# Kernel optimization log

Measured on AMD Instinct MI355X. Metric: run time of the kernel, lower is better.

Reference implementation:

```python
import jax, jax.numpy as jnp
import numpy as np
from functools import partial

TAU = 2.0
V_TH = 1.0
ALPHA = 2.0  # spikingjelly surrogate.ATan default alpha
EPS = 1e-5   # nn.LayerNorm default eps

@jax.custom_vjp
def atan_spike(v):
    # Heaviside forward; ATan surrogate gradient in bwd.
    return (v >= 0.0).astype(v.dtype)

def _atan_fwd(v):
    return atan_spike(v), v

def _atan_bwd(v, g):
    sg = (ALPHA / 2.0) / (1.0 + (jnp.pi / 2.0 * ALPHA * v) ** 2)
    return (g * sg,)

atan_spike.defvjp(_atan_fwd, _atan_bwd)

def lif_multi_step(x):
    # x: [B, T, H]; LIF with decay_input=True, v_reset=0 (hard reset), detach_reset=True.
    xt = jnp.swapaxes(x, 0, 1)  # [T, B, H]
    v0 = jnp.zeros(x.shape[:1] + x.shape[2:], dtype=x.dtype)  # reset_net per call
    def step(v, x_t):
        v = v + (x_t - v) / TAU            # charge
        s = atan_spike(v - V_TH)           # fire (surrogate grad)
        v = v * (1.0 - jax.lax.stop_gradient(s))  # hard reset to 0, detached spike
        return v, s
    _, spikes = jax.lax.scan(step, v0, xt)
    return jnp.swapaxes(spikes, 0, 1)  # [B, T, H]

def layer_norm(x, gamma, beta):
    mu = jnp.mean(x, axis=-1, keepdims=True)
    var = jnp.mean((x - mu) ** 2, axis=-1, keepdims=True)
    return (x - mu) * jax.lax.rsqrt(var + EPS) * gamma + beta

def setup_inputs() -> dict:
    key = jax.random.key(0)
    ks = jax.random.split(key, 5)
    B, T, D, H = 64, 1024, 256, 512
    x = jax.random.normal(ks[0], (B, T, D), dtype=jnp.float32)
    sc1 = 1.0 / np.sqrt(D)
    sc2 = 1.0 / np.sqrt(H)
    W1 = jax.random.uniform(ks[1], (H, D), jnp.float32, -sc1, sc1)
    b1 = jax.random.uniform(ks[2], (H,), jnp.float32, -sc1, sc1)
    W2 = jax.random.uniform(ks[3], (D, H), jnp.float32, -sc2, sc2)
    b2 = jax.random.uniform(ks[4], (D,), jnp.float32, -sc2, sc2)
    g1 = jnp.ones((H,), jnp.float32); be1 = jnp.zeros((H,), jnp.float32)
    g2 = jnp.ones((D,), jnp.float32); be2 = jnp.zeros((D,), jnp.float32)
    return {"x": x, "W1": W1, "b1": b1, "g1": g1, "be1": be1,
            "W2": W2, "b2": b2, "g2": g2, "be2": be2}

def reference(x, W1, b1, g1, be1, W2, b2, g2, be2):
    residual = x
    h = jnp.einsum('btd,hd->bth', x, W1) + b1   # fc1
    h = layer_norm(h, g1, be1)                   # norm1
    h = lif_multi_step(h)                        # lif1 (dropout = identity, eval)
    y = jnp.einsum('bth,dh->btd', h, W2) + b2    # fc2
    y = layer_norm(y, g2, be2)                   # norm2
    y = lif_multi_step(y)                        # lif2
    return residual + y
```

## Files before the change

kernel.cpp:

```cpp
#include <hip/hip_runtime.h>

typedef int v4i  __attribute__((ext_vector_type(4)));
typedef int v16i __attribute__((ext_vector_type(16)));

#define TT 1024
#define DD 256
#define HH 512
#define CB 32
#define CM (CB*TT)

__device__ __forceinline__ double shfl_xor_d(double x, int m) {
    union { double d; int u[2]; } a; a.d = x;
    a.u[0] = __shfl_xor(a.u[0], m);
    a.u[1] = __shfl_xor(a.u[1], m);
    return a.d;
}

__global__ __launch_bounds__(256) void prep_w_k(const float* __restrict__ W1,
                                                const float* __restrict__ W2,
                                                signed char* __restrict__ W1p,
                                                signed char* __restrict__ W2p) {
    int i = blockIdx.x * 256 + threadIdx.x;
    {
        double a = (double)W1[i];
        double inv = 1024.0, s = 1.0 / 1024.0;
#pragma unroll
        for (int p = 0; p < 5; ++p) {
            int d = (int)(a * inv);
            a -= d * s;
            W1p[(size_t)p * 131072 + i] = (signed char)d;
            inv *= 128.0; s *= (1.0 / 128.0);
        }
    }
    {
        double a = (double)W2[i];
        double inv = 1024.0, s = 1.0 / 1024.0;
#pragma unroll
        for (int p = 0; p < 5; ++p) {
            int d = (int)(a * inv);
            a -= d * s;
            W2p[(size_t)p * 131072 + i] = (signed char)d;
            inv *= 128.0; s *= (1.0 / 128.0);
        }
    }
}

__global__ __launch_bounds__(256) void split_x_k(const float* __restrict__ xc,
                                                 signed char* __restrict__ Xp) {
    int gid = blockIdx.x * 256 + threadIdx.x;
    int e0 = gid * 4;
    float4 xv = *(const float4*)(xc + e0);
    float fa[4] = {xv.x, xv.y, xv.z, xv.w};
    int dg[4][5];
#pragma unroll
    for (int e = 0; e < 4; ++e) {
        double a = (double)fa[e];
        double inv = 8.0, s = 0.125;
#pragma unroll
        for (int p = 0; p < 5; ++p) {
            int d = (int)(a * inv);
            a -= d * s;
            dg[e][p] = d;
            inv *= 128.0; s *= (1.0 / 128.0);
        }
    }
#pragma unroll
    for (int p = 0; p < 5; ++p) {
        int pk = (dg[0][p] & 255) | ((dg[1][p] & 255) << 8) |
                 ((dg[2][p] & 255) << 16) | ((dg[3][p] & 255) << 24);
        *(int*)(Xp + (size_t)p * ((size_t)CM * 256) + e0) = pk;
    }
}

__global__ __launch_bounds__(512, 2) void gemm1_i8(
    const signed char* __restrict__ Xp, const signed char* __restrict__ W1p,
    const float* __restrict__ b1, const float* __restrict__ g1,
    const float* __restrict__ be1, double* __restrict__ Hn) {
    __shared__ signed char Asm[5 * 32 * 256];
    __shared__ signed char Bsm[2][512 * 80];
    __shared__ double RS[8][32], RQ[8][32];
    __shared__ double MUs[32], IVs[32];

    const int tid = threadIdx.x;
    const int wave = tid >> 6, lane = tid & 63, lrow = lane & 31, lhalf = lane >> 5;
    const int m0 = blockIdx.x * 32;

    v16i acc[5][2];
#pragma unroll
    for (int g = 0; g < 5; ++g)
#pragma unroll
        for (int nt = 0; nt < 2; ++nt)
#pragma unroll
            for (int r = 0; r < 16; ++r) acc[g][nt][r] = 0;

#pragma unroll
    for (int t = 0; t < 5; ++t) {
        int idx = tid + t * 512;
        int p = idx >> 9, r = (idx >> 4) & 31, k16 = (idx & 15) << 4;
        v4i v = *(const v4i*)(Xp + (size_t)p * ((size_t)CM * 256) +
                              (size_t)(m0 + r) * 256 + k16);
        *(v4i*)&Asm[p * 8192 + r * 256 + (k16 ^ ((r & 7) << 4))] = v;
    }

    v4i breg[4];
    {
        const signed char* bp = W1p + (size_t)tid * 256;
#pragma unroll
        for (int q = 0; q < 4; ++q) breg[q] = *(const v4i*)(bp + q * 16);
    }

#pragma unroll
    for (int j = 0; j < 5; ++j) {
#pragma unroll
        for (int kk = 0; kk < 4; ++kk) {
            const int it = j * 4 + kk, bb = it & 1;
            __syncthreads();
#pragma unroll
            for (int q = 0; q < 4; ++q)
                *(v4i*)&Bsm[bb][tid * 80 + ((q * 16) ^ ((tid & 3) << 4))] = breg[q];
            __syncthreads();
            if (it < 19) {
                const int nj = (kk == 3) ? j + 1 : j;
                const int nkk = (kk == 3) ? 0 : kk + 1;
                const signed char* bp = W1p + (size_t)nj * 131072 +
                                        (size_t)tid * 256 + nkk * 64;
#pragma unroll
                for (int q = 0; q < 4; ++q) breg[q] = *(const v4i*)(bp + q * 16);
            }
            v4i bf[2][2];
#pragma unroll
            for (int nt = 0; nt < 2; ++nt)
#pragma unroll
                for (int ks = 0; ks < 2; ++ks) {
                    int hcol = wave * 64 + nt * 32 + lrow;
                    int kl = ks * 32 + lhalf * 16;
                    bf[nt][ks] = *(const v4i*)&Bsm[bb][hcol * 80 + (kl ^ ((hcol & 3) << 4))];
                }
#pragma unroll
            for (int i = 0; i <= 4 - j; ++i) {
                v4i af[2];
#pragma unroll
                for (int ks = 0; ks < 2; ++ks) {
                    int k = kk * 64 + ks * 32 + lhalf * 16;
                    af[ks] = *(const v4i*)&Asm[i * 8192 + lrow * 256 + (k ^ ((lrow & 7) << 4))];
                }
#pragma unroll
                for (int nt = 0; nt < 2; ++nt)
#pragma unroll
                    for (int ks = 0; ks < 2; ++ks)
                        acc[i + j][nt] = __builtin_amdgcn_mfma_i32_32x32x32_i8(
                            af[ks], bf[nt][ks], acc[i + j][nt], 0, 0, 0);
            }
        }
    }

    const double scl[5] = {0x1p-13, 0x1p-20, 0x1p-27, 0x1p-34, 0x1p-41};
    double vv[2][16];
    int colc[2];
#pragma unroll
    for (int nt = 0; nt < 2; ++nt) {
        colc[nt] = wave * 64 + nt * 32 + lrow;
        double bcol = (double)b1[colc[nt]];
#pragma unroll
        for (int r = 0; r < 16; ++r) {
            double t = 0.0;
#pragma unroll
            for (int g = 0; g < 5; ++g) t = fma((double)acc[g][nt][r], scl[g], t);
            vv[nt][r] = t + bcol;
        }
    }
    double ps[16], pq[16];
#pragma unroll
    for (int r = 0; r < 16; ++r) {
        ps[r] = vv[0][r] + vv[1][r];
        pq[r] = vv[0][r] * vv[0][r] + vv[1][r] * vv[1][r];
    }
#pragma unroll
    for (int m = 1; m < 32; m <<= 1)
#pragma unroll
        for (int r = 0; r < 16; ++r) {
            ps[r] += shfl_xor_d(ps[r], m);
            pq[r] += shfl_xor_d(pq[r], m);
        }
    if (lrow == 0) {
#pragma unroll
        for (int r = 0; r < 16; ++r) {
            int rw = (r & 3) + 8 * (r >> 2) + 4 * lhalf;
            RS[wave][rw] = ps[r];
            RQ[wave][rw] = pq[r];
        }
    }
    __syncthreads();
    if (tid < 32) {
        double s = 0.0, q = 0.0;
#pragma unroll
        for (int w = 0; w < 8; ++w) { s += RS[w][tid]; q += RQ[w][tid]; }
        double mu = s * (1.0 / 512.0);
        double var = q * (1.0 / 512.0) - mu * mu;
        MUs[tid] = mu;
        IVs[tid] = 1.0 / sqrt(var + 1e-5);
    }
    __syncthreads();
#pragma unroll
    for (int nt = 0; nt < 2; ++nt) {
        int col = colc[nt];
        double gg = (double)g1[col], bb2 = (double)be1[col];
#pragma unroll
        for (int r = 0; r < 16; ++r) {
            int rw = (r & 3) + 8 * (r >> 2) + 4 * lhalf;
            double o = (vv[nt][r] - MUs[rw]) * IVs[rw] * gg + bb2;
            Hn[(size_t)(m0 + rw) * 512 + col] = o;
        }
    }
}

__global__ __launch_bounds__(512, 2) void gemm2_i8(
    const signed char* __restrict__ S, const signed char* __restrict__ W2p,
    const float* __restrict__ b2, const float* __restrict__ g2,
    const float* __restrict__ be2, double* __restrict__ Yn) {
    __shared__ signed char Asm[64 * 512];
    __shared__ signed char Bsm[2][256 * 144];
    __shared__ double RS[4][64], RQ[4][64];
    __shared__ double MUs[64], IVs[64];

    const int tid = threadIdx.x;
    const int wave = tid >> 6, lane = tid & 63, lrow = lane & 31, lhalf = lane >> 5;
    const int wm = wave >> 2, wn = wave & 3;
    const int m0 = blockIdx.x * 64;

    v16i acc[5][2];
#pragma unroll
    for (int g = 0; g < 5; ++g)
#pragma unroll
        for (int nt = 0; nt < 2; ++nt)
#pragma unroll
            for (int r = 0; r < 16; ++r) acc[g][nt][r] = 0;

    {
        int r = tid >> 3, k0 = (tid & 7) * 64;
#pragma unroll
        for (int q = 0; q < 4; ++q) {
            int k = k0 + q * 16;
            v4i v = *(const v4i*)(S + (size_t)(m0 + r) * 512 + k);
            *(v4i*)&Asm[r * 512 + (k ^ ((r & 7) << 4))] = v;
        }
    }

    v4i breg[4];
    {
        const signed char* bp = W2p + (size_t)(tid >> 1) * 512 + (tid & 1) * 64;
#pragma unroll
        for (int q = 0; q < 4; ++q) breg[q] = *(const v4i*)(bp + q * 16);
    }

#pragma unroll
    for (int j = 0; j < 5; ++j) {
#pragma unroll
        for (int kk = 0; kk < 4; ++kk) {
            const int it = j * 4 + kk, bb = it & 1;
            const int d = tid >> 1, klb = (tid & 1) * 64;
            __syncthreads();
#pragma unroll
            for (int q = 0; q < 4; ++q) {
                int kl = klb + q * 16;
                *(v4i*)&Bsm[bb][d * 144 + (kl ^ ((d & 7) << 4))] = breg[q];
            }
            __syncthreads();
            if (it < 19) {
                const int nj = (kk == 3) ? j + 1 : j;
                const int nkk = (kk == 3) ? 0 : kk + 1;
                const signed char* bp = W2p + (size_t)nj * 131072 +
                                        (size_t)(tid >> 1) * 512 + nkk * 128 + (tid & 1) * 64;
#pragma unroll
                for (int q = 0; q < 4; ++q) breg[q] = *(const v4i*)(bp + q * 16);
            }
            v4i bf[2][4];
#pragma unroll
            for (int nt = 0; nt < 2; ++nt)
#pragma unroll
                for (int ks = 0; ks < 4; ++ks) {
                    int dcol = wn * 64 + nt * 32 + lrow;
                    int kl = ks * 32 + lhalf * 16;
                    bf[nt][ks] = *(const v4i*)&Bsm[bb][dcol * 144 + (kl ^ ((dcol & 7) << 4))];
                }
            v4i af[4];
#pragma unroll
            for (int ks = 0; ks < 4; ++ks) {
                int arow = wm * 32 + lrow;
                int k = kk * 128 + ks * 32 + lhalf * 16;
                af[ks] = *(const v4i*)&Asm[arow * 512 + (k ^ ((arow & 7) << 4))];
            }
#pragma unroll
            for (int nt = 0; nt < 2; ++nt)
#pragma unroll
                for (int ks = 0; ks < 4; ++ks)
                    acc[j][nt] = __builtin_amdgcn_mfma_i32_32x32x32_i8(
                        af[ks], bf[nt][ks], acc[j][nt], 0, 0, 0);
        }
    }

    const double scl[5] = {0x1p-10, 0x1p-17, 0x1p-24, 0x1p-31, 0x1p-38};
    double vv[2][16];
    int colc[2];
#pragma unroll
    for (int nt = 0; nt < 2; ++nt) {
        colc[nt] = wn * 64 + nt * 32 + lrow;
        double bcol = (double)b2[colc[nt]];
#pragma unroll
        for (int r = 0; r < 16; ++r) {
            double t = 0.0;
#pragma unroll
            for (int g = 0; g < 5; ++g) t = fma((double)acc[g][nt][r], scl[g], t);
            vv[nt][r] = t + bcol;
        }
    }
    double ps[16], pq[16];
#pragma unroll
    for (int r = 0; r < 16; ++r) {
        ps[r] = vv[0][r] + vv[1][r];
        pq[r] = vv[0][r] * vv[0][r] + vv[1][r] * vv[1][r];
    }
#pragma unroll
    for (int m = 1; m < 32; m <<= 1)
#pragma unroll
        for (int r = 0; r < 16; ++r) {
            ps[r] += shfl_xor_d(ps[r], m);
            pq[r] += shfl_xor_d(pq[r], m);
        }
    if (lrow == 0) {
#pragma unroll
        for (int r = 0; r < 16; ++r) {
            int rw = wm * 32 + (r & 3) + 8 * (r >> 2) + 4 * lhalf;
            RS[wn][rw] = ps[r];
            RQ[wn][rw] = pq[r];
        }
    }
    __syncthreads();
    if (tid < 64) {
        double s = 0.0, q = 0.0;
#pragma unroll
        for (int w = 0; w < 4; ++w) { s += RS[w][tid]; q += RQ[w][tid]; }
        double mu = s * (1.0 / 256.0);
        double var = q * (1.0 / 256.0) - mu * mu;
        MUs[tid] = mu;
        IVs[tid] = 1.0 / sqrt(var + 1e-5);
    }
    __syncthreads();
#pragma unroll
    for (int nt = 0; nt < 2; ++nt) {
        int col = colc[nt];
        double gg = (double)g2[col], bb2 = (double)be2[col];
#pragma unroll
        for (int r = 0; r < 16; ++r) {
            int rw = wm * 32 + (r & 3) + 8 * (r >> 2) + 4 * lhalf;
            double o = (vv[nt][r] - MUs[rw]) * IVs[rw] * gg + bb2;
            Yn[(size_t)(m0 + rw) * 256 + col] = o;
        }
    }
}

__global__ __launch_bounds__(64) void lif1_k(const double* __restrict__ Hn,
                                             signed char* __restrict__ S) {
    int b = blockIdx.x >> 3;
    int h = (blockIdx.x & 7) * 64 + threadIdx.x;
    const double* src = Hn + (size_t)b * TT * HH + h;
    signed char* dst = S + (size_t)b * TT * HH + h;
    double v = 0.0;
    double buf[4][16];
#pragma unroll
    for (int gg = 0; gg < 3; ++gg)
#pragma unroll
        for (int t = 0; t < 16; ++t) buf[gg][t] = src[(size_t)(gg * 16 + t) * HH];
    for (int g4 = 0; g4 < 64; g4 += 4) {
#pragma unroll
        for (int u = 0; u < 4; ++u) {
            int g = g4 + u;
            if (g + 3 < 64) {
#pragma unroll
                for (int t = 0; t < 16; ++t)
                    buf[(u + 3) & 3][t] = src[(size_t)((g + 3) * 16 + t) * HH];
            }
#pragma unroll
            for (int t = 0; t < 16; ++t) {
                v += (buf[u][t] - v) * 0.5;
                bool sp = (v >= 1.0);
                dst[(size_t)(g * 16 + t) * HH] = sp ? 1 : 0;
                if (sp) v = 0.0;
            }
        }
    }
}

__global__ __launch_bounds__(64) void lif2_k(const double* __restrict__ Yn,
                                             const float* __restrict__ X,
                                             float* __restrict__ out) {
    int b = blockIdx.x >> 2;
    int d = (blockIdx.x & 3) * 64 + threadIdx.x;
    const double* src = Yn + (size_t)b * TT * DD + d;
    const float* xs = X + (size_t)b * TT * DD + d;
    float* dst = out + (size_t)b * TT * DD + d;
    double v = 0.0;
    double bufy[4][16];
    float bufx[4][16];
#pragma unroll
    for (int gg = 0; gg < 3; ++gg)
#pragma unroll
        for (int t = 0; t < 16; ++t) {
            bufy[gg][t] = src[(size_t)(gg * 16 + t) * DD];
            bufx[gg][t] = xs[(size_t)(gg * 16 + t) * DD];
        }
    for (int g4 = 0; g4 < 64; g4 += 4) {
#pragma unroll
        for (int u = 0; u < 4; ++u) {
            int g = g4 + u;
            if (g + 3 < 64) {
#pragma unroll
                for (int t = 0; t < 16; ++t) {
                    bufy[(u + 3) & 3][t] = src[(size_t)((g + 3) * 16 + t) * DD];
                    bufx[(u + 3) & 3][t] = xs[(size_t)((g + 3) * 16 + t) * DD];
                }
            }
#pragma unroll
            for (int t = 0; t < 16; ++t) {
                v += (bufy[u][t] - v) * 0.5;
                bool sp = (v >= 1.0);
                dst[(size_t)(g * 16 + t) * DD] = bufx[u][t] + (sp ? 1.0f : 0.0f);
                if (sp) v = 0.0;
            }
        }
    }
}

extern "C" void kernel_launch(void* const* d_in, const int* in_sizes, int n_in,
                              void* d_out, int out_size, void* d_ws, size_t ws_size,
                              hipStream_t stream) {
    const float* x   = (const float*)d_in[0];
    const float* W1  = (const float*)d_in[1];
    const float* b1  = (const float*)d_in[2];
    const float* g1  = (const float*)d_in[3];
    const float* be1 = (const float*)d_in[4];
    const float* W2  = (const float*)d_in[5];
    const float* b2  = (const float*)d_in[6];
    const float* g2  = (const float*)d_in[7];
    const float* be2 = (const float*)d_in[8];
    float* out = (float*)d_out;

    char* ws = (char*)d_ws;
    signed char* W1p = (signed char*)ws;
    signed char* W2p = (signed char*)(ws + (1ull << 20));
    signed char* Xp  = (signed char*)(ws + (2ull << 20));
    double*      Yn  = (double*)(ws + (2ull << 20));
    double*      Hn  = (double*)(ws + (66ull << 20));
    signed char* Sb  = (signed char*)(ws + (194ull << 20));

    prep_w_k<<<dim3(512), dim3(256), 0, stream>>>(W1, W2, W1p, W2p);

    for (int c = 0; c < 2; ++c) {
        const float* xc = x + (size_t)c * CM * DD;
        float* outc = out + (size_t)c * CM * DD;
        split_x_k<<<dim3(8192), dim3(256), 0, stream>>>(xc, Xp);
        gemm1_i8<<<dim3(CM / 32), dim3(512), 0, stream>>>(Xp, W1p, b1, g1, be1, Hn);
        lif1_k<<<dim3(CB * 8), dim3(64), 0, stream>>>(Hn, Sb);
        gemm2_i8<<<dim3(CM / 64), dim3(512), 0, stream>>>(Sb, W2p, b2, g2, be2, Yn);
        lif2_k<<<dim3(CB * 4), dim3(64), 0, stream>>>(Yn, xc, outc);
    }
}
```

Baseline: 663.6 us.

## Fuse x digit split into gemm1 and load B fragments directly from global

```diff
diff --git a/kernel.cpp b/kernel.cpp
--- a/kernel.cpp
+++ b/kernel.cpp
@@ -45,39 +45,11 @@
     }
 }
 
-__global__ __launch_bounds__(256) void split_x_k(const float* __restrict__ xc,
-                                                 signed char* __restrict__ Xp) {
-    int gid = blockIdx.x * 256 + threadIdx.x;
-    int e0 = gid * 4;
-    float4 xv = *(const float4*)(xc + e0);
-    float fa[4] = {xv.x, xv.y, xv.z, xv.w};
-    int dg[4][5];
-#pragma unroll
-    for (int e = 0; e < 4; ++e) {
-        double a = (double)fa[e];
-        double inv = 8.0, s = 0.125;
-#pragma unroll
-        for (int p = 0; p < 5; ++p) {
-            int d = (int)(a * inv);
-            a -= d * s;
-            dg[e][p] = d;
-            inv *= 128.0; s *= (1.0 / 128.0);
-        }
-    }
-#pragma unroll
-    for (int p = 0; p < 5; ++p) {
-        int pk = (dg[0][p] & 255) | ((dg[1][p] & 255) << 8) |
-                 ((dg[2][p] & 255) << 16) | ((dg[3][p] & 255) << 24);
-        *(int*)(Xp + (size_t)p * ((size_t)CM * 256) + e0) = pk;
-    }
-}
-
 __global__ __launch_bounds__(512, 2) void gemm1_i8(
-    const signed char* __restrict__ Xp, const signed char* __restrict__ W1p,
+    const float* __restrict__ X, const signed char* __restrict__ W1p,
     const float* __restrict__ b1, const float* __restrict__ g1,
     const float* __restrict__ be1, double* __restrict__ Hn) {
-    __shared__ signed char Asm[5 * 32 * 256];
-    __shared__ signed char Bsm[2][512 * 80];
+    __shared__ signed char Asm[5 * 8192];
     __shared__ double RS[8][32], RQ[8][32];
     __shared__ double MUs[32], IVs[32];
 
@@ -85,6 +57,37 @@
     const int wave = tid >> 6, lane = tid & 63, lrow = lane & 31, lhalf = lane >> 5;
     const int m0 = blockIdx.x * 32;
 
+    {
+        const int r = tid >> 4;
+        const int k0 = (tid & 15) * 16;
+        const float* xp = X + (size_t)(m0 + r) * DD + k0;
+        float xe[16];
+        *(float4*)(xe + 0)  = *(const float4*)(xp + 0);
+        *(float4*)(xe + 4)  = *(const float4*)(xp + 4);
+        *(float4*)(xe + 8)  = *(const float4*)(xp + 8);
+        *(float4*)(xe + 12) = *(const float4*)(xp + 12);
+        int pk[5][4];
+#pragma unroll
+        for (int q = 0; q < 4; ++q)
+#pragma unroll
+            for (int e = 0; e < 4; ++e) {
+                float a = xe[q * 4 + e];
+                float inv = 8.0f, s = 0.125f;
+#pragma unroll
+                for (int p = 0; p < 5; ++p) {
+                    int d = (int)(a * inv);
+                    a -= (float)d * s;
+                    int byte = (d & 255) << (8 * e);
+                    if (e == 0) pk[p][q] = byte; else pk[p][q] |= byte;
+                    inv *= 128.0f; s *= (1.0f / 128.0f);
+                }
+            }
+        const int swz = k0 ^ ((r & 7) << 4);
+#pragma unroll
+        for (int p = 0; p < 5; ++p)
+            *(v4i*)&Asm[p * 8192 + r * 256 + swz] = *(const v4i*)pk[p];
+    }
+
     v16i acc[5][2];
 #pragma unroll
     for (int g = 0; g < 5; ++g)
@@ -93,66 +96,53 @@
 #pragma unroll
             for (int r = 0; r < 16; ++r) acc[g][nt][r] = 0;
 
-#pragma unroll
-    for (int t = 0; t < 5; ++t) {
-        int idx = tid + t * 512;
-        int p = idx >> 9, r = (idx >> 4) & 31, k16 = (idx & 15) << 4;
-        v4i v = *(const v4i*)(Xp + (size_t)p * ((size_t)CM * 256) +
-                              (size_t)(m0 + r) * 256 + k16);
-        *(v4i*)&Asm[p * 8192 + r * 256 + (k16 ^ ((r & 7) << 4))] = v;
-    }
-
-    v4i breg[4];
-    {
-        const signed char* bp = W1p + (size_t)tid * 256;
-#pragma unroll
-        for (int q = 0; q < 4; ++q) breg[q] = *(const v4i*)(bp + q * 16);
-    }
-
-#pragma unroll
-    for (int j = 0; j < 5; ++j) {
+    const signed char* bb[2];
+    bb[0] = W1p + (size_t)(wave * 64 + lrow) * 256 + lhalf * 16;
+    bb[1] = bb[0] + 32 * 256;
+
+    v4i cb[2][2];
+#pragma unroll
+    for (int nt = 0; nt < 2; ++nt)
+#pragma unroll
+        for (int ks = 0; ks < 2; ++ks)
+            cb[nt][ks] = *(const v4i*)(bb[nt] + ks * 32);
+
+    __syncthreads();
+
+    const int aswz = (lrow & 7) << 4;
+#pragma unroll
+    for (int j = 0; j < 5; ++j)
 #pragma unroll
         for (int kk = 0; kk < 4; ++kk) {
-            const int it = j * 4 + kk, bb = it & 1;
-            __syncthreads();
-#pragma unroll
-            for (int q = 0; q < 4; ++q)
-                *(v4i*)&Bsm[bb][tid * 80 + ((q * 16) ^ ((tid & 3) << 4))] = breg[q];
-            __syncthreads();
+            const int it = j * 4 + kk;
+            v4i nb[2][2];
             if (it < 19) {
                 const int nj = (kk == 3) ? j + 1 : j;
                 const int nkk = (kk == 3) ? 0 : kk + 1;
-                const signed char* bp = W1p + (size_t)nj * 131072 +
-                                        (size_t)tid * 256 + nkk * 64;
-#pragma unroll
-                for (int q = 0; q < 4; ++q) breg[q] = *(const v4i*)(bp + q * 16);
-            }
-            v4i bf[2][2];
+                const size_t off = (size_t)nj * 131072 + nkk * 64;
+#pragma unroll
+                for (int nt = 0; nt < 2; ++nt)
+#pragma unroll
+                    for (int ks = 0; ks < 2; ++ks)
+                        nb[nt][ks] = *(const v4i*)(bb[nt] + off + ks * 32);
+            }
+#pragma unroll
+            for (int i = 0; i + j < 5; ++i) {
+                v4i a0 = *(const v4i*)&Asm[i * 8192 + lrow * 256 +
+                                           ((kk * 64 + lhalf * 16) ^ aswz)];
+                v4i a1 = *(const v4i*)&Asm[i * 8192 + lrow * 256 +
+                                           ((kk * 64 + 32 + lhalf * 16) ^ aswz)];
+                acc[i + j][0] = __builtin_amdgcn_mfma_i32_32x32x32_i8(a0, cb[0][0], acc[i + j][0], 0, 0, 0);
+                acc[i + j][0] = __builtin_amdgcn_mfma_i32_32x32x32_i8(a1, cb[0][1], acc[i + j][0], 0, 0, 0);
+                acc[i + j][1] = __builtin_amdgcn_mfma_i32_32x32x32_i8(a0, cb[1][0], acc[i + j][1], 0, 0, 0);
+                acc[i + j][1] = __builtin_amdgcn_mfma_i32_32x32x32_i8(a1, cb[1][1], acc[i + j][1], 0, 0, 0);
+            }
 #pragma unroll
             for (int nt = 0; nt < 2; ++nt)
 #pragma unroll
-                for (int ks = 0; ks < 2; ++ks) {
-                    int hcol = wave * 64 + nt * 32 + lrow;
-                    int kl = ks * 32 + lhalf * 16;
-                    bf[nt][ks] = *(const v4i*)&Bsm[bb][hcol * 80 + (kl ^ ((hcol & 3) << 4))];
-                }
-#pragma unroll
-            for (int i = 0; i <= 4 - j; ++i) {
-                v4i af[2];
-#pragma unroll
-                for (int ks = 0; ks < 2; ++ks) {
-                    int k = kk * 64 + ks * 32 + lhalf * 16;
-                    af[ks] = *(const v4i*)&Asm[i * 8192 + lrow * 256 + (k ^ ((lrow & 7) << 4))];
-                }
-#pragma unroll
-                for (int nt = 0; nt < 2; ++nt)
-#pragma unroll
-                    for (int ks = 0; ks < 2; ++ks)
-                        acc[i + j][nt] = __builtin_amdgcn_mfma_i32_32x32x32_i8(
-                            af[ks], bf[nt][ks], acc[i + j][nt], 0, 0, 0);
-            }
-        }
-    }
+                for (int ks = 0; ks < 2; ++ks)
+                    cb[nt][ks] = nb[nt][ks];
+        }
 
     const double scl[5] = {0x1p-13, 0x1p-20, 0x1p-27, 0x1p-34, 0x1p-41};
     double vv[2][16];
@@ -219,7 +209,6 @@
     const float* __restrict__ b2, const float* __restrict__ g2,
     const float* __restrict__ be2, double* __restrict__ Yn) {
     __shared__ signed char Asm[64 * 512];
-    __shared__ signed char Bsm[2][256 * 144];
     __shared__ double RS[4][64], RQ[4][64];
     __shared__ double MUs[64], IVs[64];
 
@@ -228,16 +217,8 @@
     const int wm = wave >> 2, wn = wave & 3;
     const int m0 = blockIdx.x * 64;
 
-    v16i acc[5][2];
-#pragma unroll
-    for (int g = 0; g < 5; ++g)
-#pragma unroll
-        for (int nt = 0; nt < 2; ++nt)
-#pragma unroll
-            for (int r = 0; r < 16; ++r) acc[g][nt][r] = 0;
-
     {
-        int r = tid >> 3, k0 = (tid & 7) * 64;
+        const int r = tid >> 3, k0 = (tid & 7) * 64;
 #pragma unroll
         for (int q = 0; q < 4; ++q) {
             int k = k0 + q * 16;
@@ -246,58 +227,58 @@
         }
     }
 
-    v4i breg[4];
-    {
-        const signed char* bp = W2p + (size_t)(tid >> 1) * 512 + (tid & 1) * 64;
-#pragma unroll
-        for (int q = 0; q < 4; ++q) breg[q] = *(const v4i*)(bp + q * 16);
-    }
-
-#pragma unroll
-    for (int j = 0; j < 5; ++j) {
+    v16i acc[5][2];
+#pragma unroll
+    for (int g = 0; g < 5; ++g)
+#pragma unroll
+        for (int nt = 0; nt < 2; ++nt)
+#pragma unroll
+            for (int r = 0; r < 16; ++r) acc[g][nt][r] = 0;
+
+    const signed char* bb[2];
+    bb[0] = W2p + (size_t)(wn * 64 + lrow) * 512 + lhalf * 16;
+    bb[1] = bb[0] + 32 * 512;
+
+    v4i cb[2][4];
+#pragma unroll
+    for (int nt = 0; nt < 2; ++nt)
+#pragma unroll
+        for (int ks = 0; ks < 4; ++ks)
+            cb[nt][ks] = *(const v4i*)(bb[nt] + ks * 32);
+
+    __syncthreads();
+
+    const int arow = wm * 32 + lrow;
+    const int aswz = (arow & 7) << 4;
+#pragma unroll
+    for (int j = 0; j < 5; ++j)
 #pragma unroll
         for (int kk = 0; kk < 4; ++kk) {
-            const int it = j * 4 + kk, bb = it & 1;
-            const int d = tid >> 1, klb = (tid & 1) * 64;
-            __syncthreads();
-#pragma unroll
-            for (int q = 0; q < 4; ++q) {
-                int kl = klb + q * 16;
-                *(v4i*)&Bsm[bb][d * 144 + (kl ^ ((d & 7) << 4))] = breg[q];
-            }
-            __syncthreads();
+            const int it = j * 4 + kk;
+            v4i nb[2][4];
             if (it < 19) {
                 const int nj = (kk == 3) ? j + 1 : j;
                 const int nkk = (kk == 3) ? 0 : kk + 1;
-                const signed char* bp = W2p + (size_t)nj * 131072 +
-                                        (size_t)(tid >> 1) * 512 + nkk * 128 + (tid & 1) * 64;
-#pragma unroll
-                for (int q = 0; q < 4; ++q) breg[q] = *(const v4i*)(bp + q * 16);
-            }
-            v4i bf[2][4];
+                const size_t off = (size_t)nj * 131072 + nkk * 128;
+#pragma unroll
+                for (int nt = 0; nt < 2; ++nt)
+#pragma unroll
+                    for (int ks = 0; ks < 4; ++ks)
+                        nb[nt][ks] = *(const v4i*)(bb[nt] + off + ks * 32);
+            }
+#pragma unroll
+            for (int ks = 0; ks < 4; ++ks) {
+                v4i a = *(const v4i*)&Asm[arow * 512 +
+                                          ((kk * 128 + ks * 32 + lhalf * 16) ^ aswz)];
+                acc[j][0] = __builtin_amdgcn_mfma_i32_32x32x32_i8(a, cb[0][ks], acc[j][0], 0, 0, 0);
+                acc[j][1] = __builtin_amdgcn_mfma_i32_32x32x32_i8(a, cb[1][ks], acc[j][1], 0, 0, 0);
+            }
 #pragma unroll
             for (int nt = 0; nt < 2; ++nt)
 #pragma unroll
-                for (int ks = 0; ks < 4; ++ks) {
-                    int dcol = wn * 64 + nt * 32 + lrow;
-                    int kl = ks * 32 + lhalf * 16;
-                    bf[nt][ks] = *(const v4i*)&Bsm[bb][dcol * 144 + (kl ^ ((dcol & 7) << 4))];
-                }
-            v4i af[4];
-#pragma unroll
-            for (int ks = 0; ks < 4; ++ks) {
-                int arow = wm * 32 + lrow;
-                int k = kk * 128 + ks * 32 + lhalf * 16;
-                af[ks] = *(const v4i*)&Asm[arow * 512 + (k ^ ((arow & 7) << 4))];
-            }
-#pragma unroll
-            for (int nt = 0; nt < 2; ++nt)
-#pragma unroll
                 for (int ks = 0; ks < 4; ++ks)
-                    acc[j][nt] = __builtin_amdgcn_mfma_i32_32x32x32_i8(
-                        af[ks], bf[nt][ks], acc[j][nt], 0, 0, 0);
-        }
-    }
+                    cb[nt][ks] = nb[nt][ks];
+        }
 
     const double scl[5] = {0x1p-10, 0x1p-17, 0x1p-24, 0x1p-31, 0x1p-38};
     double vv[2][16];
@@ -448,18 +429,16 @@
     char* ws = (char*)d_ws;
     signed char* W1p = (signed char*)ws;
     signed char* W2p = (signed char*)(ws + (1ull << 20));
-    signed char* Xp  = (signed char*)(ws + (2ull << 20));
-    double*      Yn  = (double*)(ws + (2ull << 20));
-    double*      Hn  = (double*)(ws + (66ull << 20));
-    signed char* Sb  = (signed char*)(ws + (194ull << 20));
+    double*      Hn  = (double*)(ws + (2ull << 20));
+    signed char* Sb  = (signed char*)(ws + (130ull << 20));
+    double*      Yn  = (double*)(ws + (146ull << 20));
 
     prep_w_k<<<dim3(512), dim3(256), 0, stream>>>(W1, W2, W1p, W2p);
 
     for (int c = 0; c < 2; ++c) {
         const float* xc = x + (size_t)c * CM * DD;
         float* outc = out + (size_t)c * CM * DD;
-        split_x_k<<<dim3(8192), dim3(256), 0, stream>>>(xc, Xp);
-        gemm1_i8<<<dim3(CM / 32), dim3(512), 0, stream>>>(Xp, W1p, b1, g1, be1, Hn);
+        gemm1_i8<<<dim3(CM / 32), dim3(512), 0, stream>>>(xc, W1p, b1, g1, be1, Hn);
         lif1_k<<<dim3(CB * 8), dim3(64), 0, stream>>>(Hn, Sb);
         gemm2_i8<<<dim3(CM / 64), dim3(512), 0, stream>>>(Sb, W2p, b2, g2, be2, Yn);
         lif2_k<<<dim3(CB * 4), dim3(64), 0, stream>>>(Yn, xc, outc);
```

New measurement: 693.5 us. 1.05x slower.
